# Kernel optimization log

Hardware: AMD Instinct MI355X
Metric: run time of the kernel (lower is better)

Reference implementation:

```python
import jax, jax.numpy as jnp
import numpy as np

LN_EPS = 1e-5
N_NODES = 100000
N_EDGES = 600000
HIDDEN = 128


def setup_inputs() -> dict:
    key = jax.random.key(0)
    ks = jax.random.split(key, 6)
    s = 1.0 / np.sqrt(HIDDEN)
    x = jax.random.normal(ks[0], (N_NODES, HIDDEN), dtype=jnp.float32)
    edge_index = jax.random.randint(ks[1], (2, N_EDGES), 0, N_NODES, dtype=jnp.int64)
    W1 = jax.random.normal(ks[2], (HIDDEN, HIDDEN), dtype=jnp.float32) * s
    b1 = jnp.zeros((HIDDEN,), dtype=jnp.float32)
    W2 = jax.random.normal(ks[3], (HIDDEN, HIDDEN), dtype=jnp.float32) * s
    b2 = jnp.zeros((HIDDEN,), dtype=jnp.float32)
    gamma = jnp.ones((HIDDEN,), dtype=jnp.float32)
    beta = jnp.zeros((HIDDEN,), dtype=jnp.float32)
    return {"x": x, "edge_index": edge_index, "W1": W1, "b1": b1,
            "W2": W2, "b2": b2, "gamma": gamma, "beta": beta}


def layer_norm(h, gamma, beta):
    mu = jnp.mean(h, axis=-1, keepdims=True)
    var = jnp.mean(jnp.square(h - mu), axis=-1, keepdims=True)
    return (h - mu) * jax.lax.rsqrt(var + LN_EPS) * gamma + beta


def reference(x, edge_index, W1, b1, W2, b2, gamma, beta):
    src, dst = edge_index[0], edge_index[1]
    # GIN aggregation (eps=0): (1+eps)*x + sum_{j in N(i)} x_j
    agg = x + jax.ops.segment_sum(x[src], dst, num_segments=x.shape[0])
    # MLP: Linear -> ReLU -> Linear
    h = jax.nn.relu(agg @ W1.T + b1) @ W2.T + b2
    h = jax.nn.relu(layer_norm(h, gamma, beta))
    # dropout is identity in eval mode
    return x + h
```

## Files before the change

### kernel.cpp

```cpp
#include <hip/hip_runtime.h>

#define H 128
#define LN_EPS 1e-5f
#define CAP 32

typedef __attribute__((ext_vector_type(8))) short bf16x8;
typedef __attribute__((ext_vector_type(4))) float f32x4;

static __device__ __forceinline__ unsigned short f2bf(float f) {
  unsigned int u = __float_as_uint(f);
  u += 0x7fffu + ((u >> 16) & 1u);
  return (unsigned short)(u >> 16);
}

static __device__ __forceinline__ unsigned int cvt_pk_bf16(float lo, float hi) {
  unsigned int r;
  asm("v_cvt_pk_bf16_f32 %0, %1, %2" : "=v"(r) : "v"(lo), "v"(hi));
  return r;
}

template <int NT>
__device__ __forceinline__ void stage_w(const float* __restrict__ W,
                                        unsigned short* lds, int tid) {
#pragma unroll
  for (int it = 0; it < 4096 / NT; it++) {
    int i = tid + it * NT;
    int o = i >> 5;
    int k = (i & 31) << 2;
    float4 w = ((const float4*)W)[i];
    int byte = (o << 8) + (k << 1);
    byte ^= (o & 7) << 4;
    ushort4 wb;
    wb.x = f2bf(w.x); wb.y = f2bf(w.y); wb.z = f2bf(w.z); wb.w = f2bf(w.w);
    *(ushort4*)((char*)lds + byte) = wb;
  }
}

__global__ void k_fill_cm(const int* __restrict__ src, const int* __restrict__ dst,
                          int* __restrict__ deg, int* __restrict__ slots,
                          int ne, int nn) {
  int e = blockIdx.x * 256 + threadIdx.x;
  if (e >= ne) return;
  int d = dst[e];
  int p = atomicAdd(&deg[d], 1);
  if (p < CAP) slots[(size_t)p * nn + d] = src[e];
}

__global__ __launch_bounds__(512, 4) void k_mlp3(
    const float* __restrict__ x,
    const int* __restrict__ deg, const int* __restrict__ slots,
    const float* __restrict__ W1, const float* __restrict__ b1,
    const float* __restrict__ W2, const float* __restrict__ b2,
    const float* __restrict__ gamma, const float* __restrict__ beta,
    float* __restrict__ out, int n_nodes) {
  __shared__ unsigned short Wlds[128 * 128];

  const int tid  = threadIdx.x;
  const int wave = tid >> 6;
  const int lane = tid & 63;
  const int l15  = lane & 15;
  const int lg   = lane >> 4;
  const int xorv = (l15 & 7) << 4;
  const int row_base = blockIdx.x * 128 + wave * 16;
  const bool active = row_base < n_nodes;

  stage_w<512>(W1, Wlds, tid);

  float a[4][8];
  if (active) {
    const int row = row_base + l15;
    const float* xr = x + (size_t)row * H + lg * 8;
#pragma unroll
    for (int ks = 0; ks < 4; ks++) {
      float4 p = *(const float4*)(xr + ks * 32);
      float4 q = *(const float4*)(xr + ks * 32 + 4);
      a[ks][0] = p.x; a[ks][1] = p.y; a[ks][2] = p.z; a[ks][3] = p.w;
      a[ks][4] = q.x; a[ks][5] = q.y; a[ks][6] = q.z; a[ks][7] = q.w;
    }
    int d = deg[row];
    d = (d > CAP) ? CAP : d;
    const int* sl = slots + row;
    const int nn = n_nodes;

    int sA = (0 < d) ? sl[0] : 0;
    int sB = (1 < d) ? sl[(size_t)1 * nn] : 0;
    int i = 0;
    for (; i + 2 <= d; i += 2) {
      const int sA2 = (i + 2 < d) ? sl[(size_t)(i + 2) * nn] : 0;
      const int sB2 = (i + 3 < d) ? sl[(size_t)(i + 3) * nn] : 0;
      const float* xA = x + (size_t)sA * H + lg * 8;
      const float* xB = x + (size_t)sB * H + lg * 8;
      float4 pa[4], qa[4], pb[4], qb[4];
#pragma unroll
      for (int ks = 0; ks < 4; ks++) {
        pa[ks] = *(const float4*)(xA + ks * 32);
        qa[ks] = *(const float4*)(xA + ks * 32 + 4);
        pb[ks] = *(const float4*)(xB + ks * 32);
        qb[ks] = *(const float4*)(xB + ks * 32 + 4);
      }
#pragma unroll
      for (int ks = 0; ks < 4; ks++) {
        a[ks][0] += pa[ks].x + pb[ks].x;
        a[ks][1] += pa[ks].y + pb[ks].y;
        a[ks][2] += pa[ks].z + pb[ks].z;
        a[ks][3] += pa[ks].w + pb[ks].w;
        a[ks][4] += qa[ks].x + qb[ks].x;
        a[ks][5] += qa[ks].y + qb[ks].y;
        a[ks][6] += qa[ks].z + qb[ks].z;
        a[ks][7] += qa[ks].w + qb[ks].w;
      }
      sA = sA2; sB = sB2;
    }
    if (i < d) {
      const float* xA = x + (size_t)sA * H + lg * 8;
#pragma unroll
      for (int ks = 0; ks < 4; ks++) {
        float4 p = *(const float4*)(xA + ks * 32);
        float4 q = *(const float4*)(xA + ks * 32 + 4);
        a[ks][0] += p.x; a[ks][1] += p.y; a[ks][2] += p.z; a[ks][3] += p.w;
        a[ks][4] += q.x; a[ks][5] += q.y; a[ks][6] += q.z; a[ks][7] += q.w;
      }
    }
  }
  __syncthreads();

  unsigned int w0[8], w1[8];
  if (active) {
    bf16x8 af[4];
#pragma unroll
    for (int ks = 0; ks < 4; ks++)
#pragma unroll
      for (int j = 0; j < 8; j++) af[ks][j] = (short)f2bf(a[ks][j]);

    f32x4 acc1[8];
#pragma unroll
    for (int n = 0; n < 8; n++) acc1[n] = (f32x4){0.f, 0.f, 0.f, 0.f};
#pragma unroll
    for (int ks = 0; ks < 4; ks++) {
      const int k0 = ks * 32 + lg * 8;
#pragma unroll
      for (int n = 0; n < 8; n++) {
        const int o = n * 16 + l15;
        bf16x8 bf = *(const bf16x8*)((const char*)Wlds +
                     ((((o << 8) + (k0 << 1))) ^ xorv));
        acc1[n] = __builtin_amdgcn_mfma_f32_16x16x32_bf16(bf, af[ks], acc1[n], 0, 0, 0);
      }
    }
#pragma unroll
    for (int n = 0; n < 8; n++) {
      const float4 bb = *(const float4*)(b1 + n * 16 + lg * 4);
      float v0 = fmaxf(acc1[n][0] + bb.x, 0.f);
      float v1 = fmaxf(acc1[n][1] + bb.y, 0.f);
      float v2 = fmaxf(acc1[n][2] + bb.z, 0.f);
      float v3 = fmaxf(acc1[n][3] + bb.w, 0.f);
      w0[n] = cvt_pk_bf16(v0, v1);
      w1[n] = cvt_pk_bf16(v2, v3);
    }
  }
  __syncthreads();

  stage_w<512>(W2, Wlds, tid);

  bf16x8 a2f[4];
  if (active) {
    const int src_lo = ((lg & 1) << 5) + l15;
    const int src_hi = src_lo + 16;
    const bool nhi = (lg & 2) != 0;
#pragma unroll
    for (int ks = 0; ks < 4; ks++) {
      unsigned int m0a = __shfl(w0[2 * ks],     src_lo);
      unsigned int m0b = __shfl(w0[2 * ks + 1], src_lo);
      unsigned int m1a = __shfl(w1[2 * ks],     src_lo);
      unsigned int m1b = __shfl(w1[2 * ks + 1], src_lo);
      unsigned int m2a = __shfl(w0[2 * ks],     src_hi);
      unsigned int m2b = __shfl(w0[2 * ks + 1], src_hi);
      unsigned int m3a = __shfl(w1[2 * ks],     src_hi);
      unsigned int m3b = __shfl(w1[2 * ks + 1], src_hi);
      union { unsigned int u[4]; bf16x8 v; } c;
      c.u[0] = nhi ? m0b : m0a;
      c.u[1] = nhi ? m1b : m1a;
      c.u[2] = nhi ? m2b : m2a;
      c.u[3] = nhi ? m3b : m3a;
      a2f[ks] = c.v;
    }
  }
  __syncthreads();

  if (!active) return;

  f32x4 acc2[8];
#pragma unroll
  for (int n = 0; n < 8; n++) acc2[n] = (f32x4){0.f, 0.f, 0.f, 0.f};
#pragma unroll
  for (int ks = 0; ks < 4; ks++) {
    const int k0 = ks * 32 + lg * 8;
#pragma unroll
    for (int n = 0; n < 8; n++) {
      const int o = n * 16 + l15;
      bf16x8 bf = *(const bf16x8*)((const char*)Wlds +
                   ((((o << 8) + (k0 << 1))) ^ xorv));
      acc2[n] = __builtin_amdgcn_mfma_f32_16x16x32_bf16(bf, a2f[ks], acc2[n], 0, 0, 0);
    }
  }

  const int row = row_base + l15;
  float sum = 0.f, ssq = 0.f;
#pragma unroll
  for (int n = 0; n < 8; n++) {
    const float4 bb = *(const float4*)(b2 + n * 16 + lg * 4);
    acc2[n][0] += bb.x; acc2[n][1] += bb.y;
    acc2[n][2] += bb.z; acc2[n][3] += bb.w;
#pragma unroll
    for (int r = 0; r < 4; r++) {
      float v = acc2[n][r];
      sum += v;
      ssq += v * v;
    }
  }
  sum += __shfl_xor(sum, 16, 64);
  sum += __shfl_xor(sum, 32, 64);
  ssq += __shfl_xor(ssq, 16, 64);
  ssq += __shfl_xor(ssq, 32, 64);
  const float mu = sum * (1.0f / H);
  const float var = ssq * (1.0f / H) - mu * mu;
  const float rs = rsqrtf(var + LN_EPS);

#pragma unroll
  for (int n = 0; n < 8; n++) {
    const int col = n * 16 + lg * 4;
    const float4 g4  = *(const float4*)(gamma + col);
    const float4 be4 = *(const float4*)(beta + col);
    const float4 x4  = *(const float4*)(x + (size_t)row * H + col);
    float4 o4;
    o4.x = x4.x + fmaxf((acc2[n][0] - mu) * rs * g4.x + be4.x, 0.f);
    o4.y = x4.y + fmaxf((acc2[n][1] - mu) * rs * g4.y + be4.y, 0.f);
    o4.z = x4.z + fmaxf((acc2[n][2] - mu) * rs * g4.z + be4.z, 0.f);
    o4.w = x4.w + fmaxf((acc2[n][3] - mu) * rs * g4.w + be4.w, 0.f);
    *(float4*)(out + (size_t)row * H + col) = o4;
  }
}

__global__ void k_count(const int* __restrict__ dst, int* __restrict__ deg, int ne) {
  int e = blockIdx.x * 256 + threadIdx.x;
  if (e < ne) atomicAdd(&deg[dst[e]], 1);
}

__global__ __launch_bounds__(256) void k_scanA(const int* __restrict__ deg,
                                               int* __restrict__ off,
                                               int* __restrict__ bsum, int n) {
  __shared__ int lds[256];
  const int t = threadIdx.x;
  const int base = blockIdx.x * 1024 + t * 4;
  int4 d = make_int4(0, 0, 0, 0);
  if (base + 3 < n) d = *(const int4*)(deg + base);
  else {
    if (base + 0 < n) d.x = deg[base + 0];
    if (base + 1 < n) d.y = deg[base + 1];
    if (base + 2 < n) d.z = deg[base + 2];
    if (base + 3 < n) d.w = deg[base + 3];
  }
  const int s0 = d.x, s1 = s0 + d.y, s2 = s1 + d.z, s3 = s2 + d.w;
  lds[t] = s3;
  __syncthreads();
  for (int ofs = 1; ofs < 256; ofs <<= 1) {
    int v = (t >= ofs) ? lds[t - ofs] : 0;
    __syncthreads();
    lds[t] += v;
    __syncthreads();
  }
  const int excl = lds[t] - s3;
  if (t == 255) bsum[blockIdx.x] = lds[t];
  int4 o;
  o.x = excl; o.y = excl + s0; o.z = excl + s1; o.w = excl + s2;
  if (base + 3 < n) *(int4*)(off + base) = o;
  else {
    if (base + 0 < n) off[base + 0] = o.x;
    if (base + 1 < n) off[base + 1] = o.y;
    if (base + 2 < n) off[base + 2] = o.z;
    if (base + 3 < n) off[base + 3] = o.w;
  }
}

__global__ __launch_bounds__(256) void k_scanC(int* __restrict__ off,
                                               int* __restrict__ cur,
                                               const int* __restrict__ bsum,
                                               int n, int ne, int nb) {
  __shared__ int lds[256];
  const int t = threadIdx.x;
  int v = (t < nb) ? bsum[t] : 0;
  lds[t] = v;
  __syncthreads();
  for (int ofs = 1; ofs < 256; ofs <<= 1) {
    int u = (t >= ofs) ? lds[t - ofs] : 0;
    __syncthreads();
    lds[t] += u;
    __syncthreads();
  }
  const int add = (blockIdx.x == 0) ? 0 : lds[blockIdx.x - 1];
  const int base = blockIdx.x * 1024 + t * 4;
#pragma unroll
  for (int j = 0; j < 4; j++) {
    int i = base + j;
    if (i < n) {
      int w = off[i] + add;
      off[i] = w;
      cur[i] = w;
    }
  }
  if (blockIdx.x == 0 && t == 0) off[n] = ne;
}

__global__ void k_fill(const int* __restrict__ src, const int* __restrict__ dst,
                       int* __restrict__ cur, int* __restrict__ eidx, int ne) {
  int e = blockIdx.x * 256 + threadIdx.x;
  if (e >= ne) return;
  int p = atomicAdd(&cur[dst[e]], 1);
  eidx[p] = src[e];
}

__global__ __launch_bounds__(512, 4) void k_mlp_csr(
    const float* __restrict__ x,
    const int* __restrict__ off, const int* __restrict__ eidx,
    const float* __restrict__ W1, const float* __restrict__ b1,
    const float* __restrict__ W2, const float* __restrict__ b2,
    const float* __restrict__ gamma, const float* __restrict__ beta,
    float* __restrict__ out, int n_nodes) {
  __shared__ unsigned short Wlds[128 * 128];
  __shared__ unsigned short tile[8][16 * 128];

  const int tid  = threadIdx.x;
  const int wave = tid >> 6;
  const int lane = tid & 63;
  const int l15  = lane & 15;
  const int lg   = lane >> 4;
  const int xorv = (l15 & 7) << 4;
  const int row_base = blockIdx.x * 128 + wave * 16;
  const bool active = row_base < n_nodes;

  stage_w<512>(W1, Wlds, tid);

  float a[4][8];
  if (active) {
    const int r = row_base + l15;
    const float* xr = x + (size_t)r * H + lg * 8;
#pragma unroll
    for (int ks = 0; ks < 4; ks++) {
      float4 p = *(const float4*)(xr + ks * 32);
      float4 q = *(const float4*)(xr + ks * 32 + 4);
      a[ks][0] = p.x; a[ks][1] = p.y; a[ks][2] = p.z; a[ks][3] = p.w;
      a[ks][4] = q.x; a[ks][5] = q.y; a[ks][6] = q.z; a[ks][7] = q.w;
    }
    int e = off[r];
    const int e1 = off[r + 1];
    int s = (e < e1) ? eidx[e] : 0;
    while (e < e1) {
      const int sn = (e + 1 < e1) ? eidx[e + 1] : 0;
      const float* xs = x + (size_t)s * H + lg * 8;
#pragma unroll
      for (int ks = 0; ks < 4; ks++) {
        float4 p = *(const float4*)(xs + ks * 32);
        float4 q = *(const float4*)(xs + ks * 32 + 4);
        a[ks][0] += p.x; a[ks][1] += p.y; a[ks][2] += p.z; a[ks][3] += p.w;
        a[ks][4] += q.x; a[ks][5] += q.y; a[ks][6] += q.z; a[ks][7] += q.w;
      }
      s = sn; ++e;
    }
  }
  __syncthreads();

  if (active) {
    bf16x8 af[4];
#pragma unroll
    for (int ks = 0; ks < 4; ks++)
#pragma unroll
      for (int j = 0; j < 8; j++) af[ks][j] = (short)f2bf(a[ks][j]);

    f32x4 acc1[8];
#pragma unroll
    for (int n = 0; n < 8; n++) acc1[n] = (f32x4){0.f, 0.f, 0.f, 0.f};
#pragma unroll
    for (int ks = 0; ks < 4; ks++) {
      const int k0 = ks * 32 + lg * 8;
#pragma unroll
      for (int n = 0; n < 8; n++) {
        const int o = n * 16 + l15;
        bf16x8 bf = *(const bf16x8*)((const char*)Wlds +
                     ((((o << 8) + (k0 << 1))) ^ xorv));
        acc1[n] = __builtin_amdgcn_mfma_f32_16x16x32_bf16(af[ks], bf, acc1[n], 0, 0, 0);
      }
    }
#pragma unroll
    for (int n = 0; n < 8; n++) {
      const int col = n * 16 + l15;
      const float bias = b1[col];
#pragma unroll
      for (int r = 0; r < 4; r++) {
        float v = fmaxf(acc1[n][r] + bias, 0.f);
        const int row = lg * 4 + r;
        int byte = (row << 8) + (col << 1);
        byte ^= (row & 7) << 4;
        *(unsigned short*)((char*)tile[wave] + byte) = f2bf(v);
      }
    }
  }
  __syncthreads();

  stage_w<512>(W2, Wlds, tid);
  __syncthreads();

  if (!active) return;

  f32x4 acc2[8];
#pragma unroll
  for (int n = 0; n < 8; n++) acc2[n] = (f32x4){0.f, 0.f, 0.f, 0.f};
#pragma unroll
  for (int ks = 0; ks < 4; ks++) {
    const int k0 = ks * 32 + lg * 8;
    const int abyte = ((l15 << 8) + (k0 << 1)) ^ xorv;
    bf16x8 a2 = *(const bf16x8*)((const char*)tile[wave] + abyte);
#pragma unroll
    for (int n = 0; n < 8; n++) {
      const int o = n * 16 + l15;
      bf16x8 bf = *(const bf16x8*)((const char*)Wlds +
                   ((((o << 8) + (k0 << 1))) ^ xorv));
      acc2[n] = __builtin_amdgcn_mfma_f32_16x16x32_bf16(a2, bf, acc2[n], 0, 0, 0);
    }
  }

  float sum[4] = {0.f, 0.f, 0.f, 0.f};
  float ssq[4] = {0.f, 0.f, 0.f, 0.f};
#pragma unroll
  for (int n = 0; n < 8; n++) {
    const int col = n * 16 + l15;
    const float bias = b2[col];
#pragma unroll
    for (int r = 0; r < 4; r++) {
      float v = acc2[n][r] + bias;
      acc2[n][r] = v; sum[r] += v; ssq[r] += v * v;
    }
  }
#pragma unroll
  for (int m = 1; m <= 8; m <<= 1) {
#pragma unroll
    for (int r = 0; r < 4; r++) {
      sum[r] += __shfl_xor(sum[r], m, 64);
      ssq[r] += __shfl_xor(ssq[r], m, 64);
    }
  }
#pragma unroll
  for (int n = 0; n < 8; n++) {
    const int col = n * 16 + l15;
    const float g = gamma[col];
    const float be = beta[col];
#pragma unroll
    for (int r = 0; r < 4; r++) {
      float mu = sum[r] * (1.0f / H);
      float var = ssq[r] * (1.0f / H) - mu * mu;
      float v = (acc2[n][r] - mu) * rsqrtf(var + LN_EPS) * g + be;
      v = fmaxf(v, 0.f);
      const size_t grow = (size_t)(row_base + lg * 4 + r);
      out[grow * H + col] = x[grow * H + col] + v;
    }
  }
}

extern "C" void kernel_launch(void* const* d_in, const int* in_sizes, int n_in,
                              void* d_out, int out_size, void* d_ws, size_t ws_size,
                              hipStream_t stream) {
  const float* x  = (const float*)d_in[0];
  const int*   ei = (const int*)d_in[1];
  const float* W1 = (const float*)d_in[2];
  const float* b1 = (const float*)d_in[3];
  const float* W2 = (const float*)d_in[4];
  const float* b2 = (const float*)d_in[5];
  const float* gm = (const float*)d_in[6];
  const float* bt = (const float*)d_in[7];
  float* out = (float*)d_out;

  const int n_nodes = in_sizes[0] / H;
  const int n_edges = in_sizes[1] / 2;
  const int* src = ei;
  const int* dst = ei + n_edges;

  const size_t slots_off = ((size_t)n_nodes + 63) & ~(size_t)63;
  const size_t need_cm = (slots_off + (size_t)CAP * n_nodes) * sizeof(int);

  if (ws_size >= need_cm) {
    int* deg   = (int*)d_ws;
    int* slots = (int*)d_ws + slots_off;

    hipMemsetAsync(deg, 0, (size_t)n_nodes * sizeof(int), stream);
    k_fill_cm<<<(n_edges + 255) / 256, 256, 0, stream>>>(
        src, dst, deg, slots, n_edges, n_nodes);
    k_mlp3<<<(n_nodes + 127) / 128, 512, 0, stream>>>(
        x, deg, slots, W1, b1, W2, b2, gm, bt, out, n_nodes);
    return;
  }

  const int NBLK = (n_nodes + 1023) / 1024;
  const size_t need_csr = ((size_t)n_nodes * 3 + 2 + 1024 + (size_t)n_edges) * sizeof(int);
  if (ws_size >= need_csr && NBLK <= 256) {
    int* deg  = (int*)d_ws;
    int* off  = deg + n_nodes;
    int* cur  = off + n_nodes + 1;
    int* bsum = cur + n_nodes;
    int* eidx = bsum + 1024;

    hipMemsetAsync(deg, 0, (size_t)n_nodes * sizeof(int), stream);
    k_count<<<(n_edges + 255) / 256, 256, 0, stream>>>(dst, deg, n_edges);
    k_scanA<<<NBLK, 256, 0, stream>>>(deg, off, bsum, n_nodes);
    k_scanC<<<NBLK, 256, 0, stream>>>(off, cur, bsum, n_nodes, n_edges, NBLK);
    k_fill<<<(n_edges + 255) / 256, 256, 0, stream>>>(src, dst, cur, eidx, n_edges);
    k_mlp_csr<<<(n_nodes + 127) / 128, 512, 0, stream>>>(
        x, off, eidx, W1, b1, W2, b2, gm, bt, out, n_nodes);
    return;
  }
}
```

Baseline: 128.9 us.

## Gather neighbor features from a bf16 copy of x built in the fill kernel

Adds a prep kernel that fuses the edge slot fill with converting x to a bf16 copy in the workspace. The main kernel then gathers neighbor rows from the bf16 copy, halving the bytes moved by the random-access aggregation. It also preloads the residual x row early instead of re-reading it in the epilogue. The cost is an extra full pass over x to write the bf16 copy, and neighbor sums lose precision before the MLP (the MLP already consumed bf16). The old path is kept as a fallback when the workspace is too small.

```diff
diff --git a/kernel.cpp b/kernel.cpp
--- a/kernel.cpp
+++ b/kernel.cpp
@@ -6,6 +6,7 @@
 
 typedef __attribute__((ext_vector_type(8))) short bf16x8;
 typedef __attribute__((ext_vector_type(4))) float f32x4;
+typedef __attribute__((ext_vector_type(8))) unsigned short u16x8;
 
 static __device__ __forceinline__ unsigned short f2bf(float f) {
   unsigned int u = __float_as_uint(f);
@@ -17,6 +18,17 @@
   unsigned int r;
   asm("v_cvt_pk_bf16_f32 %0, %1, %2" : "=v"(r) : "v"(lo), "v"(hi));
   return r;
+}
+
+static __device__ __forceinline__ void acc_bf8(float* a8, const uint4 v) {
+  a8[0] += __uint_as_float(v.x << 16);
+  a8[1] += __uint_as_float(v.x & 0xffff0000u);
+  a8[2] += __uint_as_float(v.y << 16);
+  a8[3] += __uint_as_float(v.y & 0xffff0000u);
+  a8[4] += __uint_as_float(v.z << 16);
+  a8[5] += __uint_as_float(v.z & 0xffff0000u);
+  a8[6] += __uint_as_float(v.w << 16);
+  a8[7] += __uint_as_float(v.w & 0xffff0000u);
 }
 
 template <int NT>
@@ -36,6 +48,29 @@
   }
 }
 
+__global__ __launch_bounds__(256) void k_prep(
+    const float* __restrict__ x, unsigned short* __restrict__ xb,
+    const int* __restrict__ src, const int* __restrict__ dst,
+    int* __restrict__ deg, int* __restrict__ slots, int ne, int nn) {
+  const int t = blockIdx.x * 256 + threadIdx.x;
+  if (t < ne) {
+    int d = dst[t];
+    int p = atomicAdd(&deg[d], 1);
+    if (p < CAP) slots[(size_t)p * nn + d] = src[t];
+  }
+  const int nc = nn * 16;
+  if (t < nc) {
+    const float4 p = ((const float4*)x)[(size_t)t * 2];
+    const float4 q = ((const float4*)x)[(size_t)t * 2 + 1];
+    u16x8 r;
+    r[0] = (unsigned short)f2bf(p.x); r[1] = (unsigned short)f2bf(p.y);
+    r[2] = (unsigned short)f2bf(p.z); r[3] = (unsigned short)f2bf(p.w);
+    r[4] = (unsigned short)f2bf(q.x); r[5] = (unsigned short)f2bf(q.y);
+    r[6] = (unsigned short)f2bf(q.z); r[7] = (unsigned short)f2bf(q.w);
+    *(u16x8*)(xb + (size_t)t * 8) = r;
+  }
+}
+
 __global__ void k_fill_cm(const int* __restrict__ src, const int* __restrict__ dst,
                           int* __restrict__ deg, int* __restrict__ slots,
                           int ne, int nn) {
@@ -46,8 +81,8 @@
   if (p < CAP) slots[(size_t)p * nn + d] = src[e];
 }
 
-__global__ __launch_bounds__(512, 4) void k_mlp3(
-    const float* __restrict__ x,
+__global__ __launch_bounds__(512, 4) void k_mlp3b(
+    const float* __restrict__ x, const unsigned short* __restrict__ xb,
     const int* __restrict__ deg, const int* __restrict__ slots,
     const float* __restrict__ W1, const float* __restrict__ b1,
     const float* __restrict__ W2, const float* __restrict__ b2,
@@ -67,6 +102,7 @@
   stage_w<512>(W1, Wlds, tid);
 
   float a[4][8];
+  float4 xres[8];
   if (active) {
     const int row = row_base + l15;
     const float* xr = x + (size_t)row * H + lg * 8;
@@ -77,10 +113,16 @@
       a[ks][0] = p.x; a[ks][1] = p.y; a[ks][2] = p.z; a[ks][3] = p.w;
       a[ks][4] = q.x; a[ks][5] = q.y; a[ks][6] = q.z; a[ks][7] = q.w;
     }
+    const float* xrr = x + (size_t)row * H + lg * 4;
+#pragma unroll
+    for (int n = 0; n < 8; n++)
+      xres[n] = *(const float4*)(xrr + n * 16);
+
     int d = deg[row];
     d = (d > CAP) ? CAP : d;
     const int* sl = slots + row;
     const int nn = n_nodes;
+    const char* xbL = (const char*)xb + lg * 16;
 
     int sA = (0 < d) ? sl[0] : 0;
     int sB = (1 < d) ? sl[(size_t)1 * nn] : 0;
@@ -88,37 +130,27 @@
     for (; i + 2 <= d; i += 2) {
       const int sA2 = (i + 2 < d) ? sl[(size_t)(i + 2) * nn] : 0;
       const int sB2 = (i + 3 < d) ? sl[(size_t)(i + 3) * nn] : 0;
-      const float* xA = x + (size_t)sA * H + lg * 8;
-      const float* xB = x + (size_t)sB * H + lg * 8;
-      float4 pa[4], qa[4], pb[4], qb[4];
+      const char* pA = xbL + (size_t)sA * 256;
+      const char* pB = xbL + (size_t)sB * 256;
+      uint4 va[4], vb[4];
 #pragma unroll
       for (int ks = 0; ks < 4; ks++) {
-        pa[ks] = *(const float4*)(xA + ks * 32);
-        qa[ks] = *(const float4*)(xA + ks * 32 + 4);
-        pb[ks] = *(const float4*)(xB + ks * 32);
-        qb[ks] = *(const float4*)(xB + ks * 32 + 4);
+        va[ks] = *(const uint4*)(pA + ks * 64);
+        vb[ks] = *(const uint4*)(pB + ks * 64);
       }
 #pragma unroll
       for (int ks = 0; ks < 4; ks++) {
-        a[ks][0] += pa[ks].x + pb[ks].x;
-        a[ks][1] += pa[ks].y + pb[ks].y;
-        a[ks][2] += pa[ks].z + pb[ks].z;
-        a[ks][3] += pa[ks].w + pb[ks].w;
-        a[ks][4] += qa[ks].x + qb[ks].x;
-        a[ks][5] += qa[ks].y + qb[ks].y;
-        a[ks][6] += qa[ks].z + qb[ks].z;
-        a[ks][7] += qa[ks].w + qb[ks].w;
+        acc_bf8(a[ks], va[ks]);
+        acc_bf8(a[ks], vb[ks]);
       }
       sA = sA2; sB = sB2;
     }
     if (i < d) {
-      const float* xA = x + (size_t)sA * H + lg * 8;
+      const char* pA = xbL + (size_t)sA * 256;
 #pragma unroll
       for (int ks = 0; ks < 4; ks++) {
-        float4 p = *(const float4*)(xA + ks * 32);
-        float4 q = *(const float4*)(xA + ks * 32 + 4);
-        a[ks][0] += p.x; a[ks][1] += p.y; a[ks][2] += p.z; a[ks][3] += p.w;
-        a[ks][4] += q.x; a[ks][5] += q.y; a[ks][6] += q.z; a[ks][7] += q.w;
+        uint4 v = *(const uint4*)(pA + ks * 64);
+        acc_bf8(a[ks], v);
       }
     }
   }
@@ -230,6 +262,200 @@
     const int col = n * 16 + lg * 4;
     const float4 g4  = *(const float4*)(gamma + col);
     const float4 be4 = *(const float4*)(beta + col);
+    const float4 x4  = xres[n];
+    float4 o4;
+    o4.x = x4.x + fmaxf((acc2[n][0] - mu) * rs * g4.x + be4.x, 0.f);
+    o4.y = x4.y + fmaxf((acc2[n][1] - mu) * rs * g4.y + be4.y, 0.f);
+    o4.z = x4.z + fmaxf((acc2[n][2] - mu) * rs * g4.z + be4.z, 0.f);
+    o4.w = x4.w + fmaxf((acc2[n][3] - mu) * rs * g4.w + be4.w, 0.f);
+    *(float4*)(out + (size_t)row * H + col) = o4;
+  }
+}
+
+__global__ __launch_bounds__(512, 4) void k_mlp3f(
+    const float* __restrict__ x,
+    const int* __restrict__ deg, const int* __restrict__ slots,
+    const float* __restrict__ W1, const float* __restrict__ b1,
+    const float* __restrict__ W2, const float* __restrict__ b2,
+    const float* __restrict__ gamma, const float* __restrict__ beta,
+    float* __restrict__ out, int n_nodes) {
+  __shared__ unsigned short Wlds[128 * 128];
+
+  const int tid  = threadIdx.x;
+  const int wave = tid >> 6;
+  const int lane = tid & 63;
+  const int l15  = lane & 15;
+  const int lg   = lane >> 4;
+  const int xorv = (l15 & 7) << 4;
+  const int row_base = blockIdx.x * 128 + wave * 16;
+  const bool active = row_base < n_nodes;
+
+  stage_w<512>(W1, Wlds, tid);
+
+  float a[4][8];
+  if (active) {
+    const int row = row_base + l15;
+    const float* xr = x + (size_t)row * H + lg * 8;
+#pragma unroll
+    for (int ks = 0; ks < 4; ks++) {
+      float4 p = *(const float4*)(xr + ks * 32);
+      float4 q = *(const float4*)(xr + ks * 32 + 4);
+      a[ks][0] = p.x; a[ks][1] = p.y; a[ks][2] = p.z; a[ks][3] = p.w;
+      a[ks][4] = q.x; a[ks][5] = q.y; a[ks][6] = q.z; a[ks][7] = q.w;
+    }
+    int d = deg[row];
+    d = (d > CAP) ? CAP : d;
+    const int* sl = slots + row;
+    const int nn = n_nodes;
+
+    int sA = (0 < d) ? sl[0] : 0;
+    int sB = (1 < d) ? sl[(size_t)1 * nn] : 0;
+    int i = 0;
+    for (; i + 2 <= d; i += 2) {
+      const int sA2 = (i + 2 < d) ? sl[(size_t)(i + 2) * nn] : 0;
+      const int sB2 = (i + 3 < d) ? sl[(size_t)(i + 3) * nn] : 0;
+      const float* xA = x + (size_t)sA * H + lg * 8;
+      const float* xB = x + (size_t)sB * H + lg * 8;
+      float4 pa[4], qa[4], pb[4], qb[4];
+#pragma unroll
+      for (int ks = 0; ks < 4; ks++) {
+        pa[ks] = *(const float4*)(xA + ks * 32);
+        qa[ks] = *(const float4*)(xA + ks * 32 + 4);
+        pb[ks] = *(const float4*)(xB + ks * 32);
+        qb[ks] = *(const float4*)(xB + ks * 32 + 4);
+      }
+#pragma unroll
+      for (int ks = 0; ks < 4; ks++) {
+        a[ks][0] += pa[ks].x + pb[ks].x;
+        a[ks][1] += pa[ks].y + pb[ks].y;
+        a[ks][2] += pa[ks].z + pb[ks].z;
+        a[ks][3] += pa[ks].w + pb[ks].w;
+        a[ks][4] += qa[ks].x + qb[ks].x;
+        a[ks][5] += qa[ks].y + qb[ks].y;
+        a[ks][6] += qa[ks].z + qb[ks].z;
+        a[ks][7] += qa[ks].w + qb[ks].w;
+      }
+      sA = sA2; sB = sB2;
+    }
+    if (i < d) {
+      const float* xA = x + (size_t)sA * H + lg * 8;
+#pragma unroll
+      for (int ks = 0; ks < 4; ks++) {
+        float4 p = *(const float4*)(xA + ks * 32);
+        float4 q = *(const float4*)(xA + ks * 32 + 4);
+        a[ks][0] += p.x; a[ks][1] += p.y; a[ks][2] += p.z; a[ks][3] += p.w;
+        a[ks][4] += q.x; a[ks][5] += q.y; a[ks][6] += q.z; a[ks][7] += q.w;
+      }
+    }
+  }
+  __syncthreads();
+
+  unsigned int w0[8], w1[8];
+  if (active) {
+    bf16x8 af[4];
+#pragma unroll
+    for (int ks = 0; ks < 4; ks++)
+#pragma unroll
+      for (int j = 0; j < 8; j++) af[ks][j] = (short)f2bf(a[ks][j]);
+
+    f32x4 acc1[8];
+#pragma unroll
+    for (int n = 0; n < 8; n++) acc1[n] = (f32x4){0.f, 0.f, 0.f, 0.f};
+#pragma unroll
+    for (int ks = 0; ks < 4; ks++) {
+      const int k0 = ks * 32 + lg * 8;
+#pragma unroll
+      for (int n = 0; n < 8; n++) {
+        const int o = n * 16 + l15;
+        bf16x8 bf = *(const bf16x8*)((const char*)Wlds +
+                     ((((o << 8) + (k0 << 1))) ^ xorv));
+        acc1[n] = __builtin_amdgcn_mfma_f32_16x16x32_bf16(bf, af[ks], acc1[n], 0, 0, 0);
+      }
+    }
+#pragma unroll
+    for (int n = 0; n < 8; n++) {
+      const float4 bb = *(const float4*)(b1 + n * 16 + lg * 4);
+      float v0 = fmaxf(acc1[n][0] + bb.x, 0.f);
+      float v1 = fmaxf(acc1[n][1] + bb.y, 0.f);
+      float v2 = fmaxf(acc1[n][2] + bb.z, 0.f);
+      float v3 = fmaxf(acc1[n][3] + bb.w, 0.f);
+      w0[n] = cvt_pk_bf16(v0, v1);
+      w1[n] = cvt_pk_bf16(v2, v3);
+    }
+  }
+  __syncthreads();
+
+  stage_w<512>(W2, Wlds, tid);
+
+  bf16x8 a2f[4];
+  if (active) {
+    const int src_lo = ((lg & 1) << 5) + l15;
+    const int src_hi = src_lo + 16;
+    const bool nhi = (lg & 2) != 0;
+#pragma unroll
+    for (int ks = 0; ks < 4; ks++) {
+      unsigned int m0a = __shfl(w0[2 * ks],     src_lo);
+      unsigned int m0b = __shfl(w0[2 * ks + 1], src_lo);
+      unsigned int m1a = __shfl(w1[2 * ks],     src_lo);
+      unsigned int m1b = __shfl(w1[2 * ks + 1], src_lo);
+      unsigned int m2a = __shfl(w0[2 * ks],     src_hi);
+      unsigned int m2b = __shfl(w0[2 * ks + 1], src_hi);
+      unsigned int m3a = __shfl(w1[2 * ks],     src_hi);
+      unsigned int m3b = __shfl(w1[2 * ks + 1], src_hi);
+      union { unsigned int u[4]; bf16x8 v; } c;
+      c.u[0] = nhi ? m0b : m0a;
+      c.u[1] = nhi ? m1b : m1a;
+      c.u[2] = nhi ? m2b : m2a;
+      c.u[3] = nhi ? m3b : m3a;
+      a2f[ks] = c.v;
+    }
+  }
+  __syncthreads();
+
+  if (!active) return;
+
+  f32x4 acc2[8];
+#pragma unroll
+  for (int n = 0; n < 8; n++) acc2[n] = (f32x4){0.f, 0.f, 0.f, 0.f};
+#pragma unroll
+  for (int ks = 0; ks < 4; ks++) {
+    const int k0 = ks * 32 + lg * 8;
+#pragma unroll
+    for (int n = 0; n < 8; n++) {
+      const int o = n * 16 + l15;
+      bf16x8 bf = *(const bf16x8*)((const char*)Wlds +
+                   ((((o << 8) + (k0 << 1))) ^ xorv));
+      acc2[n] = __builtin_amdgcn_mfma_f32_16x16x32_bf16(bf, a2f[ks], acc2[n], 0, 0, 0);
+    }
+  }
+
+  const int row = row_base + l15;
+  float sum = 0.f, ssq = 0.f;
+#pragma unroll
+  for (int n = 0; n < 8; n++) {
+    const float4 bb = *(const float4*)(b2 + n * 16 + lg * 4);
+    acc2[n][0] += bb.x; acc2[n][1] += bb.y;
+    acc2[n][2] += bb.z; acc2[n][3] += bb.w;
+#pragma unroll
+    for (int r = 0; r < 4; r++) {
+      float v = acc2[n][r];
+      sum += v;
+      ssq += v * v;
+    }
+  }
+  sum += __shfl_xor(sum, 16, 64);
+  sum += __shfl_xor(sum, 32, 64);
+  ssq += __shfl_xor(ssq, 16, 64);
+  ssq += __shfl_xor(ssq, 32, 64);
+  const float mu = sum * (1.0f / H);
+  const float var = ssq * (1.0f / H) - mu * mu;
+  const float rs = rsqrtf(var + LN_EPS);
+
+#pragma unroll
+  for (int n = 0; n < 8; n++) {
+    const int col = n * 16 + lg * 4;
+    const float4 g4  = *(const float4*)(gamma + col);
+    const float4 be4 = *(const float4*)(beta + col);
     const float4 x4  = *(const float4*)(x + (size_t)row * H + col);
     float4 o4;
     o4.x = x4.x + fmaxf((acc2[n][0] - mu) * rs * g4.x + be4.x, 0.f);
@@ -483,7 +709,24 @@
   const int* dst = ei + n_edges;
 
   const size_t slots_off = ((size_t)n_nodes + 63) & ~(size_t)63;
-  const size_t need_cm = (slots_off + (size_t)CAP * n_nodes) * sizeof(int);
+  const size_t xb_off    = slots_off + (size_t)CAP * n_nodes;
+  const size_t need_bf   = (xb_off + (size_t)n_nodes * 64) * sizeof(int);
+  const size_t need_cm   = xb_off * sizeof(int);
+
+  if (ws_size >= need_bf) {
+    int* deg   = (int*)d_ws;
+    int* slots = (int*)d_ws + slots_off;
+    unsigned short* xb = (unsigned short*)((int*)d_ws + xb_off);
+
+    hipMemsetAsync(deg, 0, (size_t)n_nodes * sizeof(int), stream);
+    const int ncast = n_nodes * 16;
+    const int work = (n_edges > ncast) ? n_edges : ncast;
+    k_prep<<<(work + 255) / 256, 256, 0, stream>>>(
+        x, xb, src, dst, deg, slots, n_edges, n_nodes);
+    k_mlp3b<<<(n_nodes + 127) / 128, 512, 0, stream>>>(
+        x, xb, deg, slots, W1, b1, W2, b2, gm, bt, out, n_nodes);
+    return;
+  }
 
   if (ws_size >= need_cm) {
     int* deg   = (int*)d_ws;
@@ -492,7 +735,7 @@
     hipMemsetAsync(deg, 0, (size_t)n_nodes * sizeof(int), stream);
     k_fill_cm<<<(n_edges + 255) / 256, 256, 0, stream>>>(
         src, dst, deg, slots, n_edges, n_nodes);
-    k_mlp3<<<(n_nodes + 127) / 128, 512, 0, stream>>>(
+    k_mlp3f<<<(n_nodes + 127) / 128, 512, 0, stream>>>(
         x, deg, slots, W1, b1, W2, b2, gm, bt, out, n_nodes);
     return;
   }
```

After: 130.7 us. Within noise of the previous version (+1.4%).

## Gather neighbor features from a bf16 copy of x built in a fused prep kernel

Applied to the files above, without the earlier changes.

Adds a prep kernel that casts x to bf16 in workspace and, in the same launch, fills the column-major neighbor slot table. The main kernel then gathers neighbor rows from the bf16 copy, which halves the bytes per random gather, and prefetches two neighbors ahead. It also keeps the residual x tile in registers instead of reloading it, uses nontemporal output stores, and lowers occupancy hints to 2. The cost is an extra full pass over x to write the bf16 copy, higher register pressure, and neighbor sums rounded to bf16 before the first matmul (which already ran in bf16). The CSR fallback path is removed.

```diff
diff --git a/kernel.cpp b/kernel.cpp
--- a/kernel.cpp
+++ b/kernel.cpp
@@ -6,6 +6,7 @@
 
 typedef __attribute__((ext_vector_type(8))) short bf16x8;
 typedef __attribute__((ext_vector_type(4))) float f32x4;
+typedef __attribute__((ext_vector_type(8))) unsigned short u16x8;
 
 static __device__ __forceinline__ unsigned short f2bf(float f) {
   unsigned int u = __float_as_uint(f);
@@ -17,6 +18,21 @@
   unsigned int r;
   asm("v_cvt_pk_bf16_f32 %0, %1, %2" : "=v"(r) : "v"(lo), "v"(hi));
   return r;
+}
+
+static __device__ __forceinline__ void nt_st_f4(float* p, f32x4 v) {
+  __builtin_nontemporal_store(v, (f32x4*)p);
+}
+
+static __device__ __forceinline__ void acc_bf8(float* a8, const uint4 v) {
+  a8[0] += __uint_as_float(v.x << 16);
+  a8[1] += __uint_as_float(v.x & 0xffff0000u);
+  a8[2] += __uint_as_float(v.y << 16);
+  a8[3] += __uint_as_float(v.y & 0xffff0000u);
+  a8[4] += __uint_as_float(v.z << 16);
+  a8[5] += __uint_as_float(v.z & 0xffff0000u);
+  a8[6] += __uint_as_float(v.w << 16);
+  a8[7] += __uint_as_float(v.w & 0xffff0000u);
 }
 
 template <int NT>
@@ -36,6 +52,33 @@
   }
 }
 
+__global__ __launch_bounds__(256) void k_prep(
+    const float* __restrict__ x, unsigned short* __restrict__ xb,
+    const int* __restrict__ src, const int* __restrict__ dst,
+    int* __restrict__ deg, int* __restrict__ slots, int ne, int nn) {
+  const int t = blockIdx.x * 256 + threadIdx.x;
+  const int nc = nn * 16;
+  const bool do_cast = t < nc;
+  const bool do_edge = t < ne;
+  int d = 0, s = 0;
+  if (do_edge) { d = dst[t]; s = src[t]; }
+  float4 p, q;
+  if (do_cast) {
+    p = ((const float4*)x)[(size_t)t * 2];
+    q = ((const float4*)x)[(size_t)t * 2 + 1];
+  }
+  if (do_cast) {
+    u16x8 r;
+    r[0] = f2bf(p.x); r[1] = f2bf(p.y); r[2] = f2bf(p.z); r[3] = f2bf(p.w);
+    r[4] = f2bf(q.x); r[5] = f2bf(q.y); r[6] = f2bf(q.z); r[7] = f2bf(q.w);
+    *(u16x8*)(xb + (size_t)t * 8) = r;
+  }
+  if (do_edge) {
+    int pos = atomicAdd(&deg[d], 1);
+    if (pos < CAP) slots[(size_t)pos * nn + d] = s;
+  }
+}
+
 __global__ void k_fill_cm(const int* __restrict__ src, const int* __restrict__ dst,
                           int* __restrict__ deg, int* __restrict__ slots,
                           int ne, int nn) {
@@ -46,8 +89,8 @@
   if (p < CAP) slots[(size_t)p * nn + d] = src[e];
 }
 
-__global__ __launch_bounds__(512, 4) void k_mlp3(
-    const float* __restrict__ x,
+__global__ __launch_bounds__(512, 2) void k_mlp3b(
+    const float* __restrict__ x, const unsigned short* __restrict__ xb,
     const int* __restrict__ deg, const int* __restrict__ slots,
     const float* __restrict__ W1, const float* __restrict__ b1,
     const float* __restrict__ W2, const float* __restrict__ b2,
@@ -67,6 +110,7 @@
   stage_w<512>(W1, Wlds, tid);
 
   float a[4][8];
+  float4 xres[8];
   if (active) {
     const int row = row_base + l15;
     const float* xr = x + (size_t)row * H + lg * 8;
@@ -77,49 +121,60 @@
       a[ks][0] = p.x; a[ks][1] = p.y; a[ks][2] = p.z; a[ks][3] = p.w;
       a[ks][4] = q.x; a[ks][5] = q.y; a[ks][6] = q.z; a[ks][7] = q.w;
     }
+    const float* xrr = x + (size_t)row * H + lg * 4;
+#pragma unroll
+    for (int n = 0; n < 8; n++)
+      xres[n] = *(const float4*)(xrr + n * 16);
+
     int d = deg[row];
     d = (d > CAP) ? CAP : d;
     const int* sl = slots + row;
     const int nn = n_nodes;
-
-    int sA = (0 < d) ? sl[0] : 0;
-    int sB = (1 < d) ? sl[(size_t)1 * nn] : 0;
+    const char* xbL = (const char*)xb + lg * 16;
+
+    int s0 = (0 < d) ? sl[0] : 0;
+    int s1 = (1 < d) ? sl[(size_t)1 * nn] : 0;
+    int s2 = (2 < d) ? sl[(size_t)2 * nn] : 0;
+    int s3 = (3 < d) ? sl[(size_t)3 * nn] : 0;
+    uint4 va[4], vb[4];
+    if (0 < d) {
+      const char* pA = xbL + (size_t)s0 * 256;
+#pragma unroll
+      for (int ks = 0; ks < 4; ks++) va[ks] = *(const uint4*)(pA + ks * 64);
+    }
+    if (1 < d) {
+      const char* pB = xbL + (size_t)s1 * 256;
+#pragma unroll
+      for (int ks = 0; ks < 4; ks++) vb[ks] = *(const uint4*)(pB + ks * 64);
+    }
     int i = 0;
     for (; i + 2 <= d; i += 2) {
-      const int sA2 = (i + 2 < d) ? sl[(size_t)(i + 2) * nn] : 0;
-      const int sB2 = (i + 3 < d) ? sl[(size_t)(i + 3) * nn] : 0;
-      const float* xA = x + (size_t)sA * H + lg * 8;
-      const float* xB = x + (size_t)sB * H + lg * 8;
-      float4 pa[4], qa[4], pb[4], qb[4];
-#pragma unroll
-      for (int ks = 0; ks < 4; ks++) {
-        pa[ks] = *(const float4*)(xA + ks * 32);
-        qa[ks] = *(const float4*)(xA + ks * 32 + 4);
-        pb[ks] = *(const float4*)(xB + ks * 32);
-        qb[ks] = *(const float4*)(xB + ks * 32 + 4);
-      }
-#pragma unroll
-      for (int ks = 0; ks < 4; ks++) {
-        a[ks][0] += pa[ks].x + pb[ks].x;
-        a[ks][1] += pa[ks].y + pb[ks].y;
-        a[ks][2] += pa[ks].z + pb[ks].z;
-        a[ks][3] += pa[ks].w + pb[ks].w;
-        a[ks][4] += qa[ks].x + qb[ks].x;
-        a[ks][5] += qa[ks].y + qb[ks].y;
-        a[ks][6] += qa[ks].z + qb[ks].z;
-        a[ks][7] += qa[ks].w + qb[ks].w;
-      }
-      sA = sA2; sB = sB2;
+      uint4 na[4], nb[4];
+      if (i + 2 < d) {
+        const char* pA = xbL + (size_t)s2 * 256;
+#pragma unroll
+        for (int ks = 0; ks < 4; ks++) na[ks] = *(const uint4*)(pA + ks * 64);
+      }
+      if (i + 3 < d) {
+        const char* pB = xbL + (size_t)s3 * 256;
+#pragma unroll
+        for (int ks = 0; ks < 4; ks++) nb[ks] = *(const uint4*)(pB + ks * 64);
+      }
+      const int ns2 = (i + 4 < d) ? sl[(size_t)(i + 4) * nn] : 0;
+      const int ns3 = (i + 5 < d) ? sl[(size_t)(i + 5) * nn] : 0;
+#pragma unroll
+      for (int ks = 0; ks < 4; ks++) acc_bf8(a[ks], va[ks]);
+      if (i + 1 < d) {
+#pragma unroll
+        for (int ks = 0; ks < 4; ks++) acc_bf8(a[ks], vb[ks]);
+      }
+#pragma unroll
+      for (int ks = 0; ks < 4; ks++) { va[ks] = na[ks]; vb[ks] = nb[ks]; }
+      s2 = ns2; s3 = ns3;
     }
     if (i < d) {
-      const float* xA = x + (size_t)sA * H + lg * 8;
-#pragma unroll
-      for (int ks = 0; ks < 4; ks++) {
-        float4 p = *(const float4*)(xA + ks * 32);
-        float4 q = *(const float4*)(xA + ks * 32 + 4);
-        a[ks][0] += p.x; a[ks][1] += p.y; a[ks][2] += p.z; a[ks][3] += p.w;
-        a[ks][4] += q.x; a[ks][5] += q.y; a[ks][6] += q.z; a[ks][7] += q.w;
-      }
+#pragma unroll
+      for (int ks = 0; ks < 4; ks++) acc_bf8(a[ks], va[ks]);
     }
   }
   __syncthreads();
@@ -230,103 +285,24 @@
     const int col = n * 16 + lg * 4;
     const float4 g4  = *(const float4*)(gamma + col);
     const float4 be4 = *(const float4*)(beta + col);
-    const float4 x4  = *(const float4*)(x + (size_t)row * H + col);
-    float4 o4;
+    const float4 x4  = xres[n];
+    f32x4 o4;
     o4.x = x4.x + fmaxf((acc2[n][0] - mu) * rs * g4.x + be4.x, 0.f);
     o4.y = x4.y + fmaxf((acc2[n][1] - mu) * rs * g4.y + be4.y, 0.f);
     o4.z = x4.z + fmaxf((acc2[n][2] - mu) * rs * g4.z + be4.z, 0.f);
     o4.w = x4.w + fmaxf((acc2[n][3] - mu) * rs * g4.w + be4.w, 0.f);
-    *(float4*)(out + (size_t)row * H + col) = o4;
-  }
-}
-
-__global__ void k_count(const int* __restrict__ dst, int* __restrict__ deg, int ne) {
-  int e = blockIdx.x * 256 + threadIdx.x;
-  if (e < ne) atomicAdd(&deg[dst[e]], 1);
-}
-
-__global__ __launch_bounds__(256) void k_scanA(const int* __restrict__ deg,
-                                               int* __restrict__ off,
-                                               int* __restrict__ bsum, int n) {
-  __shared__ int lds[256];
-  const int t = threadIdx.x;
-  const int base = blockIdx.x * 1024 + t * 4;
-  int4 d = make_int4(0, 0, 0, 0);
-  if (base + 3 < n) d = *(const int4*)(deg + base);
-  else {
-    if (base + 0 < n) d.x = deg[base + 0];
-    if (base + 1 < n) d.y = deg[base + 1];
-    if (base + 2 < n) d.z = deg[base + 2];
-    if (base + 3 < n) d.w = deg[base + 3];
-  }
-  const int s0 = d.x, s1 = s0 + d.y, s2 = s1 + d.z, s3 = s2 + d.w;
-  lds[t] = s3;
-  __syncthreads();
-  for (int ofs = 1; ofs < 256; ofs <<= 1) {
-    int v = (t >= ofs) ? lds[t - ofs] : 0;
-    __syncthreads();
-    lds[t] += v;
-    __syncthreads();
-  }
-  const int excl = lds[t] - s3;
-  if (t == 255) bsum[blockIdx.x] = lds[t];
-  int4 o;
-  o.x = excl; o.y = excl + s0; o.z = excl + s1; o.w = excl + s2;
-  if (base + 3 < n) *(int4*)(off + base) = o;
-  else {
-    if (base + 0 < n) off[base + 0] = o.x;
-    if (base + 1 < n) off[base + 1] = o.y;
-    if (base + 2 < n) off[base + 2] = o.z;
-    if (base + 3 < n) off[base + 3] = o.w;
-  }
-}
-
-__global__ __launch_bounds__(256) void k_scanC(int* __restrict__ off,
-                                               int* __restrict__ cur,
-                                               const int* __restrict__ bsum,
-                                               int n, int ne, int nb) {
-  __shared__ int lds[256];
-  const int t = threadIdx.x;
-  int v = (t < nb) ? bsum[t] : 0;
-  lds[t] = v;
-  __syncthreads();
-  for (int ofs = 1; ofs < 256; ofs <<= 1) {
-    int u = (t >= ofs) ? lds[t - ofs] : 0;
-    __syncthreads();
-    lds[t] += u;
-    __syncthreads();
-  }
-  const int add = (blockIdx.x == 0) ? 0 : lds[blockIdx.x - 1];
-  const int base = blockIdx.x * 1024 + t * 4;
-#pragma unroll
-  for (int j = 0; j < 4; j++) {
-    int i = base + j;
-    if (i < n) {
-      int w = off[i] + add;
-      off[i] = w;
-      cur[i] = w;
-    }
-  }
-  if (blockIdx.x == 0 && t == 0) off[n] = ne;
-}
-
-__global__ void k_fill(const int* __restrict__ src, const int* __restrict__ dst,
-                       int* __restrict__ cur, int* __restrict__ eidx, int ne) {
-  int e = blockIdx.x * 256 + threadIdx.x;
-  if (e >= ne) return;
-  int p = atomicAdd(&cur[dst[e]], 1);
-  eidx[p] = src[e];
-}
-
-__global__ __launch_bounds__(512, 4) void k_mlp_csr(
+    nt_st_f4(out + (size_t)row * H + col, o4);
+  }
+}
+
+__global__ __launch_bounds__(512, 4) void k_mlp3f(
     const float* __restrict__ x,
-    const int* __restrict__ off, const int* __restrict__ eidx,
+    const int* __restrict__ deg, const int* __restrict__ slots,
     const float* __restrict__ W1, const float* __restrict__ b1,
     const float* __restrict__ W2, const float* __restrict__ b2,
     const float* __restrict__ gamma, const float* __restrict__ beta,
     float* __restrict__ out, int n_nodes) {
   __shared__ unsigned short Wlds[128 * 128];
-  __shared__ unsigned short tile[8][16 * 128];
 
   const int tid  = threadIdx.x;
   const int wave = tid >> 6;
@@ -341,8 +317,8 @@
 
   float a[4][8];
   if (active) {
-    const int r = row_base + l15;
-    const float* xr = x + (size_t)r * H + lg * 8;
+    const int row = row_base + l15;
+    const float* xr = x + (size_t)row * H + lg * 8;
 #pragma unroll
     for (int ks = 0; ks < 4; ks++) {
       float4 p = *(const float4*)(xr + ks * 32);
@@ -350,24 +326,54 @@
       a[ks][0] = p.x; a[ks][1] = p.y; a[ks][2] = p.z; a[ks][3] = p.w;
       a[ks][4] = q.x; a[ks][5] = q.y; a[ks][6] = q.z; a[ks][7] = q.w;
     }
-    int e = off[r];
-    const int e1 = off[r + 1];
-    int s = (e < e1) ? eidx[e] : 0;
-    while (e < e1) {
-      const int sn = (e + 1 < e1) ? eidx[e + 1] : 0;
-      const float* xs = x + (size_t)s * H + lg * 8;
+    int d = deg[row];
+    d = (d > CAP) ? CAP : d;
+    const int* sl = slots + row;
+    const int nn = n_nodes;
+
+    int sA = (0 < d) ? sl[0] : 0;
+    int sB = (1 < d) ? sl[(size_t)1 * nn] : 0;
+    int i = 0;
+    for (; i + 2 <= d; i += 2) {
+      const int sA2 = (i + 2 < d) ? sl[(size_t)(i + 2) * nn] : 0;
+      const int sB2 = (i + 3 < d) ? sl[(size_t)(i + 3) * nn] : 0;
+      const float* xA = x + (size_t)sA * H + lg * 8;
+      const float* xB = x + (size_t)sB * H + lg * 8;
+      float4 pa[4], qa[4], pb[4], qb[4];
 #pragma unroll
       for (int ks = 0; ks < 4; ks++) {
-        float4 p = *(const float4*)(xs + ks * 32);
-        float4 q = *(const float4*)(xs + ks * 32 + 4);
+        pa[ks] = *(const float4*)(xA + ks * 32);
+        qa[ks] = *(const float4*)(xA + ks * 32 + 4);
+        pb[ks] = *(const float4*)(xB + ks * 32);
+        qb[ks] = *(const float4*)(xB + ks * 32 + 4);
+      }
+#pragma unroll
+      for (int ks = 0; ks < 4; ks++) {
+        a[ks][0] += pa[ks].x + pb[ks].x;
+        a[ks][1] += pa[ks].y + pb[ks].y;
+        a[ks][2] += pa[ks].z + pb[ks].z;
+        a[ks][3] += pa[ks].w + pb[ks].w;
+        a[ks][4] += qa[ks].x + qb[ks].x;
+        a[ks][5] += qa[ks].y + qb[ks].y;
+        a[ks][6] += qa[ks].z + qb[ks].z;
+        a[ks][7] += qa[ks].w + qb[ks].w;
+      }
+      sA = sA2; sB = sB2;
+    }
+    if (i < d) {
+      const float* xA = x + (size_t)sA * H + lg * 8;
+#pragma unroll
+      for (int ks = 0; ks < 4; ks++) {
+        float4 p = *(const float4*)(xA + ks * 32);
+        float4 q = *(const float4*)(xA + ks * 32 + 4);
         a[ks][0] += p.x; a[ks][1] += p.y; a[ks][2] += p.z; a[ks][3] += p.w;
         a[ks][4] += q.x; a[ks][5] += q.y; a[ks][6] += q.z; a[ks][7] += q.w;
       }
-      s = sn; ++e;
     }
   }
   __syncthreads();
 
+  unsigned int w0[8], w1[8];
   if (active) {
     bf16x8 af[4];
 #pragma unroll
@@ -386,26 +392,47 @@
         const int o = n * 16 + l15;
         bf16x8 bf = *(const bf16x8*)((const char*)Wlds +
                      ((((o << 8) + (k0 << 1))) ^ xorv));
-        acc1[n] = __builtin_amdgcn_mfma_f32_16x16x32_bf16(af[ks], bf, acc1[n], 0, 0, 0);
+        acc1[n] = __builtin_amdgcn_mfma_f32_16x16x32_bf16(bf, af[ks], acc1[n], 0, 0, 0);
       }
     }
 #pragma unroll
     for (int n = 0; n < 8; n++) {
-      const int col = n * 16 + l15;
-      const float bias = b1[col];
-#pragma unroll
-      for (int r = 0; r < 4; r++) {
-        float v = fmaxf(acc1[n][r] + bias, 0.f);
-        const int row = lg * 4 + r;
-        int byte = (row << 8) + (col << 1);
-        byte ^= (row & 7) << 4;
-        *(unsigned short*)((char*)tile[wave] + byte) = f2bf(v);
-      }
+      const float4 bb = *(const float4*)(b1 + n * 16 + lg * 4);
+      float v0 = fmaxf(acc1[n][0] + bb.x, 0.f);
+      float v1 = fmaxf(acc1[n][1] + bb.y, 0.f);
+      float v2 = fmaxf(acc1[n][2] + bb.z, 0.f);
+      float v3 = fmaxf(acc1[n][3] + bb.w, 0.f);
+      w0[n] = cvt_pk_bf16(v0, v1);
+      w1[n] = cvt_pk_bf16(v2, v3);
     }
   }
   __syncthreads();
 
   stage_w<512>(W2, Wlds, tid);
+
+  bf16x8 a2f[4];
+  if (active) {
+    const int src_lo = ((lg & 1) << 5) + l15;
+    const int src_hi = src_lo + 16;
+    const bool nhi = (lg & 2) != 0;
+#pragma unroll
+    for (int ks = 0; ks < 4; ks++) {
+      unsigned int m0a = __shfl(w0[2 * ks],     src_lo);
+      unsigned int m0b = __shfl(w0[2 * ks + 1], src_lo);
+      unsigned int m1a = __shfl(w1[2 * ks],     src_lo);
+      unsigned int m1b = __shfl(w1[2 * ks + 1], src_lo);
+      unsigned int m2a = __shfl(w0[2 * ks],     src_hi);
+      unsigned int m2b = __shfl(w0[2 * ks + 1], src_hi);
+      unsigned int m3a = __shfl(w1[2 * ks],     src_hi);
+      unsigned int m3b = __shfl(w1[2 * ks + 1], src_hi);
+      union { unsigned int u[4]; bf16x8 v; } c;
+      c.u[0] = nhi ? m0b : m0a;
+      c.u[1] = nhi ? m1b : m1a;
+      c.u[2] = nhi ? m2b : m2a;
+      c.u[3] = nhi ? m3b : m3a;
+      a2f[ks] = c.v;
+    }
+  }
   __syncthreads();
 
   if (!active) return;
@@ -416,51 +443,49 @@
 #pragma unroll
   for (int ks = 0; ks < 4; ks++) {
     const int k0 = ks * 32 + lg * 8;
-    const int abyte = ((l15 << 8) + (k0 << 1)) ^ xorv;
-    bf16x8 a2 = *(const bf16x8*)((const char*)tile[wave] + abyte);
 #pragma unroll
     for (int n = 0; n < 8; n++) {
       const int o = n * 16 + l15;
       bf16x8 bf = *(const bf16x8*)((const char*)Wlds +
                    ((((o << 8) + (k0 << 1))) ^ xorv));
-      acc2[n] = __builtin_amdgcn_mfma_f32_16x16x32_bf16(a2, bf, acc2[n], 0, 0, 0);
-    }
-  }
-
-  float sum[4] = {0.f, 0.f, 0.f, 0.f};
-  float ssq[4] = {0.f, 0.f, 0.f, 0.f};
+      acc2[n] = __builtin_amdgcn_mfma_f32_16x16x32_bf16(bf, a2f[ks], acc2[n], 0, 0, 0);
+    }
+  }
+
+  const int row = row_base + l15;
+  float sum = 0.f, ssq = 0.f;
 #pragma unroll
   for (int n = 0; n < 8; n++) {
-    const int col = n * 16 + l15;
-    const float bias = b2[col];
+    const float4 bb = *(const float4*)(b2 + n * 16 + lg * 4);
+    acc2[n][0] += bb.x; acc2[n][1] += bb.y;
+    acc2[n][2] += bb.z; acc2[n][3] += bb.w;
 #pragma unroll
     for (int r = 0; r < 4; r++) {
-      float v = acc2[n][r] + bias;
-      acc2[n][r] = v; sum[r] += v; ssq[r] += v * v;
-    }
-  }
-#pragma unroll
-  for (int m = 1; m <= 8; m <<= 1) {
-#pragma unroll
-    for (int r = 0; r < 4; r++) {
-      sum[r] += __shfl_xor(sum[r], m, 64);
-      ssq[r] += __shfl_xor(ssq[r], m, 64);
-    }
-  }
+      float v = acc2[n][r];
+      sum += v;
+      ssq += v * v;
+    }
+  }
+  sum += __shfl_xor(sum, 16, 64);
+  sum += __shfl_xor(sum, 32, 64);
+  ssq += __shfl_xor(ssq, 16, 64);
+  ssq += __shfl_xor(ssq, 32, 64);
+  const float mu = sum * (1.0f / H);
+  const float var = ssq * (1.0f / H) - mu * mu;
+  const float rs = rsqrtf(var + LN_EPS);
+
 #pragma unroll
   for (int n = 0; n < 8; n++) {
-    const int col = n * 16 + l15;
-    const float g = gamma[col];
-    const float be = beta[col];
-#pragma unroll
-    for (int r = 0; r < 4; r++) {
-      float mu = sum[r] * (1.0f / H);
-      float var = ssq[r] * (1.0f / H) - mu * mu;
-      float v = (acc2[n][r] - mu) * rsqrtf(var + LN_EPS) * g + be;
-      v = fmaxf(v, 0.f);
-      const size_t grow = (size_t)(row_base + lg * 4 + r);
-      out[grow * H + col] = x[grow * H + col] + v;
-    }
+    const int col = n * 16 + lg * 4;
+    const float4 g4  = *(const float4*)(gamma + col);
+    const float4 be4 = *(const float4*)(beta + col);
+    const float4 x4  = *(const float4*)(x + (size_t)row * H + col);
+    float4 o4;
+    o4.x = x4.x + fmaxf((acc2[n][0] - mu) * rs * g4.x + be4.x, 0.f);
+    o4.y = x4.y + fmaxf((acc2[n][1] - mu) * rs * g4.y + be4.y, 0.f);
+    o4.z = x4.z + fmaxf((acc2[n][2] - mu) * rs * g4.z + be4.z, 0.f);
+    o4.w = x4.w + fmaxf((acc2[n][3] - mu) * rs * g4.w + be4.w, 0.f);
+    *(float4*)(out + (size_t)row * H + col) = o4;
   }
 }
 
@@ -483,7 +508,24 @@
   const int* dst = ei + n_edges;
 
   const size_t slots_off = ((size_t)n_nodes + 63) & ~(size_t)63;
-  const size_t need_cm = (slots_off + (size_t)CAP * n_nodes) * sizeof(int);
+  const size_t xb_off    = slots_off + (size_t)CAP * n_nodes;
+  const size_t need_bf   = (xb_off + (size_t)n_nodes * 64) * sizeof(int);
+  const size_t need_cm   = xb_off * sizeof(int);
+
+  if (ws_size >= need_bf) {
+    int* deg   = (int*)d_ws;
+    int* slots = (int*)d_ws + slots_off;
+    unsigned short* xb = (unsigned short*)((int*)d_ws + xb_off);
+
+    hipMemsetAsync(deg, 0, (size_t)n_nodes * sizeof(int), stream);
+    const int ncast = n_nodes * 16;
+    const int work = (n_edges > ncast) ? n_edges : ncast;
+    k_prep<<<(work + 255) / 256, 256, 0, stream>>>(
+        x, xb, src, dst, deg, slots, n_edges, n_nodes);
+    k_mlp3b<<<(n_nodes + 127) / 128, 512, 0, stream>>>(
+        x, xb, deg, slots, W1, b1, W2, b2, gm, bt, out, n_nodes);
+    return;
+  }
 
   if (ws_size >= need_cm) {
     int* deg   = (int*)d_ws;
@@ -492,27 +534,8 @@
     hipMemsetAsync(deg, 0, (size_t)n_nodes * sizeof(int), stream);
     k_fill_cm<<<(n_edges + 255) / 256, 256, 0, stream>>>(
         src, dst, deg, slots, n_edges, n_nodes);
-    k_mlp3<<<(n_nodes + 127) / 128, 512, 0, stream>>>(
+    k_mlp3f<<<(n_nodes + 127) / 128, 512, 0, stream>>>(
         x, deg, slots, W1, b1, W2, b2, gm, bt, out, n_nodes);
     return;
   }
-
-  const int NBLK = (n_nodes + 1023) / 1024;
-  const size_t need_csr = ((size_t)n_nodes * 3 + 2 + 1024 + (size_t)n_edges) * sizeof(int);
-  if (ws_size >= need_csr && NBLK <= 256) {
-    int* deg  = (int*)d_ws;
-    int* off  = deg + n_nodes;
-    int* cur  = off + n_nodes + 1;
-    int* bsum = cur + n_nodes;
-    int* eidx = bsum + 1024;
-
-    hipMemsetAsync(deg, 0, (size_t)n_nodes * sizeof(int), stream);
-    k_count<<<(n_edges + 255) / 256, 256, 0, stream>>>(dst, deg, n_edges);
-    k_scanA<<<NBLK, 256, 0, stream>>>(deg, off, bsum, n_nodes);
-    k_scanC<<<NBLK, 256, 0, stream>>>(off, cur, bsum, n_nodes, n_edges, NBLK);
-    k_fill<<<(n_edges + 255) / 256, 256, 0, stream>>>(src, dst, cur, eidx, n_edges);
-    k_mlp_csr<<<(n_nodes + 127) / 128, 512, 0, stream>>>(
-        x, off, eidx, W1, b1, W2, b2, gm, bt, out, n_nodes);
-    return;
-  }
-}
+}
```

After: 124.4 us. -3.5%, faster.
